# Kernel optimization log

Hardware: AMD Instinct MI355X
Metric: run time of the kernel (lower is better)

Reference implementation:

```python
import jax, jax.numpy as jnp
import numpy as np

NUM_CLASSES = 21
THRESH = 0.5
NEG_POS = 3
VAR0, VAR1 = 0.1, 0.2


def point_form(boxes):
    # center form (cx,cy,w,h) -> corner form (x1,y1,x2,y2)
    return jnp.concatenate([boxes[:, :2] - boxes[:, 2:] / 2,
                            boxes[:, :2] + boxes[:, 2:] / 2], axis=1)


def jaccard(a, b):
    # a: [N,4] corner form, b: [P,4] corner form -> IoU [N,P]
    lt = jnp.maximum(a[:, None, :2], b[None, :, :2])
    rb = jnp.minimum(a[:, None, 2:], b[None, :, 2:])
    wh = jnp.clip(rb - lt, 0.0)
    inter = wh[..., 0] * wh[..., 1]
    area_a = (a[:, 2] - a[:, 0]) * (a[:, 3] - a[:, 1])
    area_b = (b[:, 2] - b[:, 0]) * (b[:, 3] - b[:, 1])
    return inter / (area_a[:, None] + area_b[None, :] - inter)


def match_one(truths, labels, priors):
    # truths: [N,4] corner form, labels: [N] int, priors: [P,4] center form
    ov = jaccard(truths, point_form(priors))            # [N,P]
    best_prior_idx = jnp.argmax(ov, axis=1)             # [N] best prior per truth
    best_truth_ov = jnp.max(ov, axis=0)                 # [P]
    best_truth_idx = jnp.argmax(ov, axis=0)             # [P]
    # ensure each truth keeps its best prior
    best_truth_ov = best_truth_ov.at[best_prior_idx].set(2.0)
    best_truth_idx = best_truth_idx.at[best_prior_idx].set(
        jnp.arange(truths.shape[0], dtype=best_truth_idx.dtype))
    matches = truths[best_truth_idx]                    # [P,4]
    conf = labels[best_truth_idx] + 1                   # [P]
    conf = jnp.where(best_truth_ov < THRESH, 0, conf)
    # encode
    g_cxcy = ((matches[:, :2] + matches[:, 2:]) / 2 - priors[:, :2]) / (VAR0 * priors[:, 2:])
    g_wh = jnp.log((matches[:, 2:] - matches[:, :2]) / priors[:, 2:]) / VAR1
    return jnp.concatenate([g_cxcy, g_wh], axis=1), conf


def setup_inputs() -> dict:
    key = jax.random.key(0)
    k1, k2, k3, k4, k5, k6, k7 = jax.random.split(key, 7)
    B, P, C, N = 64, 24564, NUM_CLASSES, 16
    loc_data = jax.random.normal(k1, (B, P, 4), dtype=jnp.float32)
    conf_data = jax.random.normal(k2, (B, P, C), dtype=jnp.float32)
    # priors: valid center-form boxes
    ctr = 0.05 + 0.9 * jax.random.uniform(k3, (P, 2), dtype=jnp.float32)
    pwh = 0.05 + 0.25 * jax.random.uniform(k4, (P, 2), dtype=jnp.float32)
    priors = jnp.concatenate([ctr, pwh], axis=1)
    # truths: valid corner-form boxes
    xy1 = 0.7 * jax.random.uniform(k5, (B, N, 2), dtype=jnp.float32)
    twh = 0.05 + 0.2 * jax.random.uniform(k6, (B, N, 2), dtype=jnp.float32)
    truths = jnp.concatenate([xy1, xy1 + twh], axis=2)
    labels = jax.random.randint(k7, (B, N), 0, 20, dtype=jnp.int32)
    return {"loc_data": loc_data, "conf_data": conf_data, "priors": priors,
            "truths": truths, "labels": labels}


def reference(loc_data, conf_data, priors, truths, labels):
    B, P, C = conf_data.shape
    loc_t, conf_t = jax.vmap(lambda t, l: match_one(t, l, priors))(truths, labels)
    pos = conf_t > 0                                     # [B,P]

    # localization smooth-L1, summed over positives
    diff = loc_data - loc_t
    ad = jnp.abs(diff)
    sl1 = jnp.where(ad < 1.0, 0.5 * diff * diff, ad - 0.5)
    loss_l = jnp.sum(sl1 * pos[..., None].astype(loc_data.dtype))

    # per-prior CE = logsumexp - logit at matched class
    lse = jax.nn.logsumexp(conf_data, axis=2)            # [B,P]
    gathered = jnp.take_along_axis(conf_data, conf_t[..., None].astype(jnp.int32), axis=2)[..., 0]
    loss_c_all = lse - gathered

    # hard-negative mining via double argsort rank (pos zeroed first)
    loss_c_mine = jnp.where(pos, 0.0, loss_c_all)
    idx_rank = jnp.argsort(jnp.argsort(-loss_c_mine, axis=1), axis=1)
    num_pos = jnp.sum(pos, axis=1, keepdims=True)        # [B,1]
    num_neg = jnp.minimum(NEG_POS * num_pos, P - 1)
    neg = idx_rank < num_neg

    mask = pos | neg
    loss_c = jnp.sum(jnp.where(mask, loss_c_all, 0.0))

    n = jnp.sum(num_pos).astype(loc_data.dtype)
    return loss_l / n, loss_c / n
```

## Files before the change

### kernel.cpp

```cpp
#include <hip/hip_runtime.h>
#include <cstdint>
#include <cstddef>

#define B_ 64
#define P_ 24564
#define C_ 21
#define N_ 16
#define NPL_ 96
#define THRESH_ 0.5f


__device__ inline void async_copy16(const float* g, float* l) {
    __builtin_amdgcn_global_load_lds(
        (const __attribute__((address_space(1))) void*)g,
        (__attribute__((address_space(3))) void*)l, 16, 0, 0);
}

__device__ inline float sl1_encode(float4 ld, float4 pr,
                                   float tx1, float ty1, float tx2, float ty2) {
    float gcx = ((tx1 + tx2) * 0.5f - pr.x) / (0.1f * pr.z);
    float gcy = ((ty1 + ty2) * 0.5f - pr.y) / (0.1f * pr.w);
    float gw  = __logf((tx2 - tx1) / pr.z) / 0.2f;
    float gh  = __logf((ty2 - ty1) / pr.w) / 0.2f;
    float g[4] = {gcx, gcy, gw, gh};
    float l[4] = {ld.x, ld.y, ld.z, ld.w};
    float s = 0.0f;
#pragma unroll
    for (int i = 0; i < 4; i++) {
        float d = l[i] - g[i];
        float ad = fabsf(d);
        s += (ad < 1.0f) ? 0.5f * d * d : ad - 0.5f;
    }
    return s;
}

__device__ inline void scan_hist(const int* h, int M, int kk,
                                 int* outB, int* outR) {
    int lane = threadIdx.x & 63;
    int CH = M >> 6;
    int base = M - (lane + 1) * CH;
    int s = 0;
    for (int j = 0; j < CH; j++) s += h[base + j];
    int incl = s;
#pragma unroll
    for (int off = 1; off < 64; off <<= 1) {
        int v = __shfl_up(incl, off);
        if (lane >= off) incl += v;
    }
    int excl = incl - s;
    if (excl < kk && excl + s >= kk) {
        int acc = excl;
        for (int bin = base + CH - 1; bin >= base; bin--) {
            int c = h[bin];
            if (acc + c >= kk) { *outB = bin; *outR = kk - acc; break; }
            acc += c;
        }
    }
}


__global__ __launch_bounds__(256, 6) void
kF_fused(const float* __restrict__ loc,
         const float* __restrict__ conf,
         const float* __restrict__ priors,
         const float* __restrict__ truths,
         const int* __restrict__ labels,
         float* __restrict__ mine,
         float* __restrict__ part_ll,
         float* __restrict__ part_pce,
         int* __restrict__ part_np,
         unsigned long long* __restrict__ part_key) {
    int b = blockIdx.y, bx = blockIdx.x, t = threadIdx.x;
    int wid = t >> 6, lane = t & 63;
    __shared__ float scf[4 * 1536];
    __shared__ unsigned long long swk[N_ * 4];
    __shared__ float sll[4], spc[4];
    __shared__ int snp[4];

    int base_p = bx * 256;
    int nvalid = min(256, P_ - base_p);
    int maxf4 = (nvalid * C_) >> 2;
    const float* gtile = conf + ((size_t)b * P_ + base_p) * C_;

    int p0 = base_p + t;
    bool valid = t < nvalid;
    float4 pr = ((const float4*)priors)[valid ? p0 : base_p];
    float px1 = pr.x - pr.z * 0.5f, py1 = pr.y - pr.w * 0.5f;
    float px2 = pr.x + pr.z * 0.5f, py2 = pr.y + pr.w * 0.5f;
    float ap = (px2 - px1) * (py2 - py1);

    float* slice = scf + wid * 1536;
    int wf4 = wid * 336;
#pragma unroll
    for (int i = 0; i < 6; i++) {
        int f4 = wf4 + i * 64 + lane;
        int s4 = (f4 < maxf4) ? f4 : (maxf4 - 1);
        async_copy16(gtile + (size_t)s4 * 4, slice + i * 256);
    }

    float best = -1.0f;
    int bn = 0, bl = 0;
#pragma unroll
    for (int n = 0; n < N_; n++) {
        float4 tb = ((const float4*)truths)[b * N_ + n];
        int ln = labels[b * N_ + n];
        float at = (tb.z - tb.x) * (tb.w - tb.y);
        float lx = fmaxf(tb.x, px1), ly = fmaxf(tb.y, py1);
        float rx = fminf(tb.z, px2), ry = fminf(tb.w, py2);
        float w = fmaxf(rx - lx, 0.0f), h = fmaxf(ry - ly, 0.0f);
        float inter = w * h;
        float iou = inter / (at + ap - inter);
        if (iou > best) { best = iou; bn = n; bl = ln; }

        unsigned k32 = valid ? __float_as_uint(iou) : 0u;
        unsigned m = k32;
#pragma unroll
        for (int off = 32; off; off >>= 1) {
            unsigned o = __shfl_xor(m, off);
            m = (o > m) ? o : m;
        }
        unsigned long long msk = __ballot(k32 == m);
        int wl = (int)__ffsll(msk) - 1;
        if (lane == 0)
            swk[n * 4 + wid] = ((unsigned long long)m << 32) |
                               (unsigned)~(unsigned)(base_p + (wid << 6) + wl);
    }
    int pos = (valid && best >= THRESH_) ? 1 : 0;

    asm volatile("s_waitcnt vmcnt(0)" ::: "memory");

    float ll = 0.0f, pce = 0.0f;
    int np = 0;
    if (valid) {
        int cls = pos ? (bl + 1) : 0;
        const float* row = scf + wid * 1536 + lane * 21;
        float ssum = 0.0f;
#pragma unroll
        for (int i = 0; i < 21; i++) ssum += __expf(row[i]);
        float g = row[cls];
        float lca = fmaxf(__logf(ssum) - g, 0.0f);

        mine[(size_t)b * P_ + p0] = pos ? 0.0f : lca;

        if (pos) {
            np = 1;
            pce = lca;
            float4 ld = ((const float4*)loc)[(size_t)b * P_ + p0];
            float4 tb = ((const float4*)truths)[b * N_ + bn];
            ll = sl1_encode(ld, pr, tb.x, tb.y, tb.z, tb.w);
        }
    }

    for (int off = 32; off; off >>= 1) {
        ll += __shfl_down(ll, off);
        pce += __shfl_down(pce, off);
        np += __shfl_down(np, off);
    }
    if (lane == 0) { sll[wid] = ll; spc[wid] = pce; snp[wid] = np; }

    __syncthreads();
    if (t < N_) {
        unsigned long long bk = swk[t * 4];
#pragma unroll
        for (int i = 1; i < 4; i++) {
            unsigned long long o = swk[t * 4 + i];
            bk = (o > bk) ? o : bk;
        }
        part_key[(size_t)(b * NPL_ + bx) * N_ + t] = bk;
    }
    if (t == 0) {
        float a = 0.0f, cc = 0.0f;
        int q = 0;
        for (int i = 0; i < 4; i++) { a += sll[i]; cc += spc[i]; q += snp[i]; }
        part_ll[b * NPL_ + bx] = a;
        part_pce[b * NPL_ + bx] = cc;
        part_np[b * NPL_ + bx] = q;
    }
}

__global__ __launch_bounds__(1024) void
kB_batch(const float* __restrict__ loc,
         const float* __restrict__ conf,
         const float* __restrict__ priors,
         const float* __restrict__ truths,
         const int* __restrict__ labels,
         const float* __restrict__ mine,
         const float* __restrict__ part_ll,
         const float* __restrict__ part_pce,
         const int* __restrict__ part_np,
         const unsigned long long* __restrict__ part_key,
         double* __restrict__ bll,
         double* __restrict__ bpc,
         int* __restrict__ bnp) {
    int b = blockIdx.x, t = threadIdx.x, wid = t >> 6, lane = t & 63;
    __shared__ float tr[N_ * 4];
    __shared__ int lb[N_];
    __shared__ unsigned long long skmax[N_];
    __shared__ int sp[N_];
    __shared__ float sdll, sdpce, sll_s, spc_s;
    __shared__ int sdnp, snp_s;
    __shared__ int hist[4 * 2048];
    __shared__ int hist2[1024];
    __shared__ int hist3[1024];
    __shared__ int sB[3], sR[3];
    __shared__ float wsum[16];
    __shared__ int wcgt[16];

    if (t < N_ * 4) tr[t] = truths[b * N_ * 4 + t];
    if (t < N_) { lb[t] = labels[b * N_ + t]; skmax[t] = 0ull; }
#pragma unroll
    for (int i = 0; i < 8; i++) hist[t + (i << 10)] = 0;
    hist2[t] = 0;
    hist3[t] = 0;
    if (t == 0) { sdll = 0.f; sdpce = 0.f; sdnp = 0; sll_s = 0.f; spc_s = 0.f; snp_s = 0; }
    __syncthreads();
    if (t < 256) {
        int n = t & 15, j = t >> 4;
        unsigned long long bk = 0ull;
        for (int i = j; i < NPL_; i += 16) {
            unsigned long long k = part_key[(size_t)(b * NPL_ + i) * N_ + n];
            bk = (k > bk) ? k : bk;
        }
        atomicMax(&skmax[n], bk);
    }
    if (t < 128) {
        float a = 0.f, c2 = 0.f;
        int q = 0;
        if (t < NPL_) {
            a = part_ll[b * NPL_ + t];
            c2 = part_pce[b * NPL_ + t];
            q = part_np[b * NPL_ + t];
        }
        for (int off = 32; off; off >>= 1) {
            a += __shfl_down(a, off);
            c2 += __shfl_down(c2, off);
            q += __shfl_down(q, off);
        }
        if (lane == 0) {
            atomicAdd(&sll_s, a);
            atomicAdd(&spc_s, c2);
            atomicAdd(&snp_s, q);
        }
    }
    __syncthreads();
    if (t < N_) sp[t] = (int)~(unsigned)(skmax[t] & 0xFFFFFFFFull);
    __syncthreads();
    if (t < N_) {
        int p = sp[t];
        bool last = true;
        for (int n = t + 1; n < N_; n++) if (sp[n] == p) last = false;
        if (last) {
            int nf = t;
            float4 pr = ((const float4*)priors)[p];
            float px1 = pr.x - pr.z * 0.5f, py1 = pr.y - pr.w * 0.5f;
            float px2 = pr.x + pr.z * 0.5f, py2 = pr.y + pr.w * 0.5f;
            float ap = (px2 - px1) * (py2 - py1);
            float best = -1.0f;
            int bti = 0;
            for (int n = 0; n < N_; n++) {
                float tx1 = tr[n * 4], ty1 = tr[n * 4 + 1];
                float tx2 = tr[n * 4 + 2], ty2 = tr[n * 4 + 3];
                float at = (tx2 - tx1) * (ty2 - ty1);
                float lx = fmaxf(tx1, px1), ly = fmaxf(ty1, py1);
                float rx = fminf(tx2, px2), ry = fminf(ty2, py2);
                float w = fmaxf(rx - lx, 0.0f), h = fmaxf(ry - ly, 0.0f);
                float inter = w * h;
                float iou = inter / (at + ap - inter);
                if (iou > best) { best = iou; bti = n; }
            }
            int pos_old = (best >= THRESH_) ? 1 : 0;
            const float* cp = conf + ((size_t)b * P_ + p) * C_;
            float ssum = 0.0f;
            for (int j = 0; j < C_; j++) ssum += __expf(cp[j]);
            float lse = __logf(ssum);
            float4 ld = ((const float4*)loc)[(size_t)b * P_ + p];
            float dll = sl1_encode(ld, pr, tr[nf * 4], tr[nf * 4 + 1],
                                   tr[nf * 4 + 2], tr[nf * 4 + 3]);
            float dpce = lse - cp[lb[nf] + 1];
            int dnp = 1 - pos_old;
            if (pos_old) {
                dll -= sl1_encode(ld, pr, tr[bti * 4], tr[bti * 4 + 1],
                                  tr[bti * 4 + 2], tr[bti * 4 + 3]);
                dpce -= lse - cp[lb[bti] + 1];
            }
            atomicAdd(&sdll, dll);
            atomicAdd(&sdpce, dpce);
            atomicAdd(&sdnp, dnp);
        }
    }

    unsigned omask = 0;
#pragma unroll
    for (int n = 0; n < N_; n++) {
        int p = sp[n];
        if ((p & 1023) == t) omask |= 1u << (p >> 10);
    }
    const float* v = mine + (size_t)b * P_;
    int nel = (t < (P_ - 23 * 1024)) ? 24 : 23;
    float xv[24];
#pragma unroll
    for (int i = 0; i < 24; i++) {
        float x = 0.0f;
        if (i < nel) x = v[t + (i << 10)];
        if ((omask >> i) & 1) x = 0.0f;
        xv[i] = x;
    }

    int rep = (wid & 3) << 11;
#pragma unroll
    for (int i = 0; i < 24; i++) {
        if (i < nel) {
            unsigned bb = __float_as_uint(xv[i]);
            atomicAdd(&hist[rep + (bb >> 20)], 1);
        }
    }
    __syncthreads();
    {
        int h0 = hist[t] + hist[t + 2048] + hist[t + 4096] + hist[t + 6144];
        int h1 = hist[t + 1024] + hist[t + 3072] + hist[t + 5120] + hist[t + 7168];
        hist[t] = h0;
        hist[t + 1024] = h1;
    }
    __syncthreads();

    int np = snp_s + sdnp;
    int k = np * 3;
    if (k > P_ - 1) k = P_ - 1;

    unsigned T = 0x7FFFFFFFu;
    if (k > 0) {
        if (wid == 0) scan_hist(hist, 2048, k, &sB[0], &sR[0]);
        __syncthreads();
        unsigned B1 = (unsigned)sB[0];
        int k1 = sR[0];
#pragma unroll
        for (int i = 0; i < 24; i++) {
            if (i < nel) {
                unsigned bb = __float_as_uint(xv[i]);
                if ((bb >> 20) == B1) atomicAdd(&hist2[(bb >> 10) & 0x3FF], 1);
            }
        }
        __syncthreads();
        if (wid == 0) scan_hist(hist2, 1024, k1, &sB[1], &sR[1]);
        __syncthreads();
        unsigned hi = (B1 << 10) | (unsigned)sB[1];
        int k2 = sR[1];
#pragma unroll
        for (int i = 0; i < 24; i++) {
            if (i < nel) {
                unsigned bb = __float_as_uint(xv[i]);
                if ((bb >> 10) == hi) atomicAdd(&hist3[bb & 0x3FF], 1);
            }
        }
        __syncthreads();
        if (wid == 0) scan_hist(hist3, 1024, k2, &sB[2], &sR[2]);
        __syncthreads();
        T = (hi << 10) | (unsigned)sB[2];
    }

    float psum = 0.0f;
    int cgt = 0;
#pragma unroll
    for (int i = 0; i < 24; i++) {
        if (__float_as_uint(xv[i]) > T) { psum += xv[i]; cgt++; }
    }
    for (int off = 32; off; off >>= 1) {
        psum += __shfl_down(psum, off);
        cgt += __shfl_down(cgt, off);
    }
    if (lane == 0) { wsum[wid] = psum; wcgt[wid] = cgt; }
    __syncthreads();
    if (t == 0) {
        float s2 = 0.0f;
        int cg = 0;
        for (int i = 0; i < 16; i++) { s2 += wsum[i]; cg += wcgt[i]; }
        int skrem = k - cg;
        double tot = (double)s2 + (double)skrem * (double)__uint_as_float(T);
        bll[b] = (double)(sll_s + sdll);
        bpc[b] = (double)(spc_s + sdpce) + tot;
        bnp[b] = np;
    }
}

__global__ void kC_final(const double* __restrict__ bll,
                         const double* __restrict__ bpc,
                         const int* __restrict__ bnp,
                         float* __restrict__ out) {
    int t = threadIdx.x;
    double a = bll[t], c = bpc[t];
    int n = bnp[t];
    for (int off = 32; off; off >>= 1) {
        a += __shfl_down(a, off);
        c += __shfl_down(c, off);
        n += __shfl_down(n, off);
    }
    if (t == 0) {
        double dn = (double)n;
        out[0] = (float)(a / dn);
        out[1] = (float)(c / dn);
    }
}


extern "C" void kernel_launch(void* const* d_in, const int* in_sizes, int n_in,
                              void* d_out, int out_size, void* d_ws, size_t ws_size,
                              hipStream_t stream) {
    const float* loc    = (const float*)d_in[0];
    const float* conf   = (const float*)d_in[1];
    const float* priors = (const float*)d_in[2];
    const float* truths = (const float*)d_in[3];
    const int*   labels = (const int*)d_in[4];
    float* out = (float*)d_out;

    char* ws = (char*)d_ws;
    unsigned long long* part_key = (unsigned long long*)(ws);
    float*  part_ll  = (float*)(ws + 786432);
    float*  part_pce = (float*)(ws + 811008);
    int*    part_np  = (int*)(ws + 835584);
    double* bll      = (double*)(ws + 860160);
    double* bpc      = (double*)(ws + 860672);
    int*    bnp      = (int*)(ws + 861184);
    float*  mine     = (float*)(ws + 1048576);

    hipLaunchKernelGGL(kF_fused, dim3(NPL_, B_), dim3(256), 0, stream,
                       loc, conf, priors, truths, labels,
                       mine, part_ll, part_pce, part_np, part_key);
    hipLaunchKernelGGL(kB_batch, dim3(B_), dim3(1024), 0, stream,
                       loc, conf, priors, truths, labels, mine,
                       part_ll, part_pce, part_np, part_key, bll, bpc, bnp);
    hipLaunchKernelGGL(kC_final, dim3(1), dim3(64), 0, stream, bll, bpc, bnp, out);
}
```

Baseline: 232.6 us.

## Defer per-truth best-prior reduction to shared-memory pass after main compute

Instead of doing 16 wave-wide max-reductions with ballot inside the IoU loop, each thread keeps its 16 IoU keys in registers and writes them to reused shared memory after the loss computation. Each wave then reduces 4 truths over the whole block using 64-bit shuffles. The label load becomes one indexed load after the loop, and the occupancy hint is dropped from launch bounds. This moves reduction work off the critical path before the LDS wait but adds an extra barrier, 16 more live registers and extra LDS traffic.

```diff
diff --git a/kernel.cpp b/kernel.cpp
--- a/kernel.cpp
+++ b/kernel.cpp
@@ -9,6 +9,13 @@
 #define NPL_ 96
 #define THRESH_ 0.5f
 
+
+__device__ inline unsigned long long shfl_down_u64(unsigned long long v, int off) {
+    unsigned lo = (unsigned)v, hi = (unsigned)(v >> 32);
+    lo = __shfl_down(lo, off);
+    hi = __shfl_down(hi, off);
+    return ((unsigned long long)hi << 32) | lo;
+}
 
 __device__ inline void async_copy16(const float* g, float* l) {
     __builtin_amdgcn_global_load_lds(
@@ -59,7 +66,7 @@
 }
 
 
-__global__ __launch_bounds__(256, 6) void
+__global__ __launch_bounds__(256) void
 kF_fused(const float* __restrict__ loc,
          const float* __restrict__ conf,
          const float* __restrict__ priors,
@@ -73,9 +80,9 @@
     int b = blockIdx.y, bx = blockIdx.x, t = threadIdx.x;
     int wid = t >> 6, lane = t & 63;
     __shared__ float scf[4 * 1536];
-    __shared__ unsigned long long swk[N_ * 4];
     __shared__ float sll[4], spc[4];
     __shared__ int snp[4];
+    unsigned* skey = (unsigned*)scf;
 
     int base_p = bx * 256;
     int nvalid = min(256, P_ - base_p);
@@ -98,34 +105,23 @@
         async_copy16(gtile + (size_t)s4 * 4, slice + i * 256);
     }
 
+    unsigned u[N_];
     float best = -1.0f;
-    int bn = 0, bl = 0;
+    int bn = 0;
 #pragma unroll
     for (int n = 0; n < N_; n++) {
         float4 tb = ((const float4*)truths)[b * N_ + n];
-        int ln = labels[b * N_ + n];
         float at = (tb.z - tb.x) * (tb.w - tb.y);
         float lx = fmaxf(tb.x, px1), ly = fmaxf(tb.y, py1);
         float rx = fminf(tb.z, px2), ry = fminf(tb.w, py2);
         float w = fmaxf(rx - lx, 0.0f), h = fmaxf(ry - ly, 0.0f);
         float inter = w * h;
         float iou = inter / (at + ap - inter);
-        if (iou > best) { best = iou; bn = n; bl = ln; }
-
-        unsigned k32 = valid ? __float_as_uint(iou) : 0u;
-        unsigned m = k32;
-#pragma unroll
-        for (int off = 32; off; off >>= 1) {
-            unsigned o = __shfl_xor(m, off);
-            m = (o > m) ? o : m;
-        }
-        unsigned long long msk = __ballot(k32 == m);
-        int wl = (int)__ffsll(msk) - 1;
-        if (lane == 0)
-            swk[n * 4 + wid] = ((unsigned long long)m << 32) |
-                               (unsigned)~(unsigned)(base_p + (wid << 6) + wl);
+        if (iou > best) { best = iou; bn = n; }
+        u[n] = valid ? __float_as_uint(iou) : 0u;
     }
     int pos = (valid && best >= THRESH_) ? 1 : 0;
+    int bl = labels[b * N_ + bn];
 
     asm volatile("s_waitcnt vmcnt(0)" ::: "memory");
 
@@ -159,14 +155,32 @@
     if (lane == 0) { sll[wid] = ll; spc[wid] = pce; snp[wid] = np; }
 
     __syncthreads();
-    if (t < N_) {
-        unsigned long long bk = swk[t * 4];
-#pragma unroll
-        for (int i = 1; i < 4; i++) {
-            unsigned long long o = swk[t * 4 + i];
+#pragma unroll
+    for (int n = 0; n < N_; n++) skey[n * 256 + t] = u[n];
+    __syncthreads();
+
+#pragma unroll
+    for (int i = 0; i < 4; i++) {
+        int n = wid + 4 * i;
+        unsigned long long bk = 0ull;
+#pragma unroll
+        for (int q = 0; q < 4; q++) {
+            int tt = lane + 64 * q;
+            unsigned k32 = skey[n * 256 + tt];
+            unsigned long long v = ((unsigned long long)k32 << 32) |
+                                   (unsigned)~(unsigned)tt;
+            bk = (v > bk) ? v : bk;
+        }
+        for (int off = 32; off; off >>= 1) {
+            unsigned long long o = shfl_down_u64(bk, off);
             bk = (o > bk) ? o : bk;
         }
-        part_key[(size_t)(b * NPL_ + bx) * N_ + t] = bk;
+        if (lane == 0) {
+            int twin = (int)~(unsigned)(bk & 0xFFFFFFFFull);
+            int pwin = base_p + twin;
+            part_key[(size_t)(b * NPL_ + bx) * N_ + n] =
+                (bk & 0xFFFFFFFF00000000ull) | (unsigned)~(unsigned)pwin;
+        }
     }
     if (t == 0) {
         float a = 0.0f, cc = 0.0f;
```

Result: no change. 235.8 us (+1.4%).

## Process two priors per thread in fused match kernel with 512-prior tiles

Applied to the files above, without the earlier changes.

Each block now handles 512 priors instead of 256, with every thread computing IoU matching and cross-entropy for two priors. The per-truth best-prior search now packs IoU and index into a 64-bit key and reduces it with a shuffle, replacing the max-shuffle plus ballot. This halves the number of blocks and partial results that the batch kernel must combine, and amortises the per-truth loads. The cost is more LDS per block (about 45 KB), higher register use and the removal of the occupancy hint, so fewer waves may be resident to hide memory latency.

```diff
diff --git a/kernel.cpp b/kernel.cpp
--- a/kernel.cpp
+++ b/kernel.cpp
@@ -6,9 +6,16 @@
 #define P_ 24564
 #define C_ 21
 #define N_ 16
-#define NPL_ 96
+#define NPL_ 48
 #define THRESH_ 0.5f
 
+
+__device__ inline unsigned long long shfl_down_u64(unsigned long long v, int off) {
+    unsigned lo = (unsigned)v, hi = (unsigned)(v >> 32);
+    lo = __shfl_down(lo, off);
+    hi = __shfl_down(hi, off);
+    return ((unsigned long long)hi << 32) | lo;
+}
 
 __device__ inline void async_copy16(const float* g, float* l) {
     __builtin_amdgcn_global_load_lds(
@@ -59,7 +66,7 @@
 }
 
 
-__global__ __launch_bounds__(256, 6) void
+__global__ __launch_bounds__(256) void
 kF_fused(const float* __restrict__ loc,
          const float* __restrict__ conf,
          const float* __restrict__ priors,
@@ -70,84 +77,115 @@
          float* __restrict__ part_pce,
          int* __restrict__ part_np,
          unsigned long long* __restrict__ part_key) {
-    int b = blockIdx.y, bx = blockIdx.x, t = threadIdx.x;
+    int b = blockIdx.y, bxi = blockIdx.x, t = threadIdx.x;
     int wid = t >> 6, lane = t & 63;
-    __shared__ float scf[4 * 1536];
+    __shared__ float scf[4 * 2816];
     __shared__ unsigned long long swk[N_ * 4];
     __shared__ float sll[4], spc[4];
     __shared__ int snp[4];
 
-    int base_p = bx * 256;
-    int nvalid = min(256, P_ - base_p);
+    int base_p = bxi * 512;
+    int nvalid = min(512, P_ - base_p);
     int maxf4 = (nvalid * C_) >> 2;
     const float* gtile = conf + ((size_t)b * P_ + base_p) * C_;
 
-    int p0 = base_p + t;
-    bool valid = t < nvalid;
-    float4 pr = ((const float4*)priors)[valid ? p0 : base_p];
-    float px1 = pr.x - pr.z * 0.5f, py1 = pr.y - pr.w * 0.5f;
-    float px2 = pr.x + pr.z * 0.5f, py2 = pr.y + pr.w * 0.5f;
-    float ap = (px2 - px1) * (py2 - py1);
-
-    float* slice = scf + wid * 1536;
-    int wf4 = wid * 336;
-#pragma unroll
-    for (int i = 0; i < 6; i++) {
+    float* slice = scf + wid * 2816;
+    int wf4 = wid * 672;
+#pragma unroll
+    for (int i = 0; i < 11; i++) {
         int f4 = wf4 + i * 64 + lane;
         int s4 = (f4 < maxf4) ? f4 : (maxf4 - 1);
         async_copy16(gtile + (size_t)s4 * 4, slice + i * 256);
     }
 
-    float best = -1.0f;
-    int bn = 0, bl = 0;
+    int r0 = (wid << 7) + lane;
+    int r1 = r0 + 64;
+    bool v0 = r0 < nvalid, v1 = r1 < nvalid;
+    float4 prA = ((const float4*)priors)[base_p + (v0 ? r0 : 0)];
+    float4 prB = ((const float4*)priors)[base_p + (v1 ? r1 : 0)];
+    float ax1 = prA.x - prA.z * 0.5f, ay1 = prA.y - prA.w * 0.5f;
+    float ax2 = prA.x + prA.z * 0.5f, ay2 = prA.y + prA.w * 0.5f;
+    float aA = (ax2 - ax1) * (ay2 - ay1);
+    float qx1 = prB.x - prB.z * 0.5f, qy1 = prB.y - prB.w * 0.5f;
+    float qx2 = prB.x + prB.z * 0.5f, qy2 = prB.y + prB.w * 0.5f;
+    float aB = (qx2 - qx1) * (qy2 - qy1);
+
+    float bestA = -1.0f, bestB = -1.0f;
+    int bnA = 0, bnB = 0;
 #pragma unroll
     for (int n = 0; n < N_; n++) {
         float4 tb = ((const float4*)truths)[b * N_ + n];
-        int ln = labels[b * N_ + n];
         float at = (tb.z - tb.x) * (tb.w - tb.y);
-        float lx = fmaxf(tb.x, px1), ly = fmaxf(tb.y, py1);
-        float rx = fminf(tb.z, px2), ry = fminf(tb.w, py2);
-        float w = fmaxf(rx - lx, 0.0f), h = fmaxf(ry - ly, 0.0f);
-        float inter = w * h;
-        float iou = inter / (at + ap - inter);
-        if (iou > best) { best = iou; bn = n; bl = ln; }
-
-        unsigned k32 = valid ? __float_as_uint(iou) : 0u;
-        unsigned m = k32;
+        float lxA = fmaxf(tb.x, ax1), lyA = fmaxf(tb.y, ay1);
+        float rxA = fminf(tb.z, ax2), ryA = fminf(tb.w, ay2);
+        float wA = fmaxf(rxA - lxA, 0.0f), hA = fmaxf(ryA - lyA, 0.0f);
+        float iA = wA * hA;
+        float iouA = iA / (at + aA - iA);
+        if (iouA > bestA) { bestA = iouA; bnA = n; }
+        float lxB = fmaxf(tb.x, qx1), lyB = fmaxf(tb.y, qy1);
+        float rxB = fminf(tb.z, qx2), ryB = fminf(tb.w, qy2);
+        float wB = fmaxf(rxB - lxB, 0.0f), hB = fmaxf(ryB - lyB, 0.0f);
+        float iB = wB * hB;
+        float iouB = iB / (at + aB - iB);
+        if (iouB > bestB) { bestB = iouB; bnB = n; }
+
+        unsigned kA = v0 ? __float_as_uint(iouA) : 0u;
+        unsigned kB2 = v1 ? __float_as_uint(iouB) : 0u;
+        unsigned long long vA = ((unsigned long long)kA << 32) |
+                                (unsigned)~(unsigned)r0;
+        unsigned long long vB = ((unsigned long long)kB2 << 32) |
+                                (unsigned)~(unsigned)r1;
+        unsigned long long bk = (vA > vB) ? vA : vB;
 #pragma unroll
         for (int off = 32; off; off >>= 1) {
-            unsigned o = __shfl_xor(m, off);
-            m = (o > m) ? o : m;
-        }
-        unsigned long long msk = __ballot(k32 == m);
-        int wl = (int)__ffsll(msk) - 1;
-        if (lane == 0)
-            swk[n * 4 + wid] = ((unsigned long long)m << 32) |
-                               (unsigned)~(unsigned)(base_p + (wid << 6) + wl);
-    }
-    int pos = (valid && best >= THRESH_) ? 1 : 0;
+            unsigned long long o = shfl_down_u64(bk, off);
+            bk = (o > bk) ? o : bk;
+        }
+        if (lane == 0) {
+            int rw = (int)~(unsigned)(bk & 0xFFFFFFFFull);
+            swk[n * 4 + wid] = (bk & 0xFFFFFFFF00000000ull) |
+                               (unsigned)~(unsigned)(base_p + rw);
+        }
+    }
+    int posA = (v0 && bestA >= THRESH_) ? 1 : 0;
+    int posB = (v1 && bestB >= THRESH_) ? 1 : 0;
+    int blA = labels[b * N_ + bnA];
+    int blB = labels[b * N_ + bnB];
 
     asm volatile("s_waitcnt vmcnt(0)" ::: "memory");
 
     float ll = 0.0f, pce = 0.0f;
     int np = 0;
-    if (valid) {
-        int cls = pos ? (bl + 1) : 0;
-        const float* row = scf + wid * 1536 + lane * 21;
+    if (v0) {
+        int cls = posA ? (blA + 1) : 0;
+        const float* rowp = slice + lane * 21;
         float ssum = 0.0f;
 #pragma unroll
-        for (int i = 0; i < 21; i++) ssum += __expf(row[i]);
-        float g = row[cls];
+        for (int i = 0; i < 21; i++) ssum += __expf(rowp[i]);
+        float g = rowp[cls];
         float lca = fmaxf(__logf(ssum) - g, 0.0f);
-
-        mine[(size_t)b * P_ + p0] = pos ? 0.0f : lca;
-
-        if (pos) {
-            np = 1;
-            pce = lca;
-            float4 ld = ((const float4*)loc)[(size_t)b * P_ + p0];
-            float4 tb = ((const float4*)truths)[b * N_ + bn];
-            ll = sl1_encode(ld, pr, tb.x, tb.y, tb.z, tb.w);
+        mine[(size_t)b * P_ + base_p + r0] = posA ? 0.0f : lca;
+        if (posA) {
+            np++; pce += lca;
+            float4 ld = ((const float4*)loc)[(size_t)b * P_ + base_p + r0];
+            float4 tb = ((const float4*)truths)[b * N_ + bnA];
+            ll += sl1_encode(ld, prA, tb.x, tb.y, tb.z, tb.w);
+        }
+    }
+    if (v1) {
+        int cls = posB ? (blB + 1) : 0;
+        const float* rowp = slice + (lane + 64) * 21;
+        float ssum = 0.0f;
+#pragma unroll
+        for (int i = 0; i < 21; i++) ssum += __expf(rowp[i]);
+        float g = rowp[cls];
+        float lca = fmaxf(__logf(ssum) - g, 0.0f);
+        mine[(size_t)b * P_ + base_p + r1] = posB ? 0.0f : lca;
+        if (posB) {
+            np++; pce += lca;
+            float4 ld = ((const float4*)loc)[(size_t)b * P_ + base_p + r1];
+            float4 tb = ((const float4*)truths)[b * N_ + bnB];
+            ll += sl1_encode(ld, prB, tb.x, tb.y, tb.z, tb.w);
         }
     }
 
@@ -166,15 +204,15 @@
             unsigned long long o = swk[t * 4 + i];
             bk = (o > bk) ? o : bk;
         }
-        part_key[(size_t)(b * NPL_ + bx) * N_ + t] = bk;
+        part_key[(size_t)(b * NPL_ + bxi) * N_ + t] = bk;
     }
     if (t == 0) {
         float a = 0.0f, cc = 0.0f;
         int q = 0;
         for (int i = 0; i < 4; i++) { a += sll[i]; cc += spc[i]; q += snp[i]; }
-        part_ll[b * NPL_ + bx] = a;
-        part_pce[b * NPL_ + bx] = cc;
-        part_np[b * NPL_ + bx] = q;
+        part_ll[b * NPL_ + bxi] = a;
+        part_pce[b * NPL_ + bxi] = cc;
+        part_np[b * NPL_ + bxi] = q;
     }
 }
 
```

Measured after the change: 246.6 us. 6.0% more time.
